# Kernel tuning notes

Hardware: AMD Instinct MI355X
Metric: run time of the kernel (lower is better)

## Reference

```python
import jax, jax.numpy as jnp
import numpy as np

HIDDEN = 1024
TYPE_SIZE = 1000
BATCH = 32
SEQLEN = 512


def setup_inputs() -> dict:
    key = jax.random.key(0)
    k1, k2, k3, k4, k5 = jax.random.split(key, 5)
    event_seqs = jax.random.randint(k1, (BATCH, SEQLEN), 0, TYPE_SIZE + 1)
    duration_seqs = jax.random.uniform(k2, (BATCH, SEQLEN), dtype=jnp.float32)
    # nn.Linear(2H, 7H): weight [7H, 2H], bias [7H]
    bound = 1.0 / np.sqrt(2 * HIDDEN)
    W_rec = jax.random.uniform(k3, (7 * HIDDEN, 2 * HIDDEN), minval=-bound, maxval=bound, dtype=jnp.float32)
    b_rec = jax.random.uniform(k4, (7 * HIDDEN,), minval=-bound, maxval=bound, dtype=jnp.float32)
    emb_table = jax.random.normal(k5, (TYPE_SIZE + 1, HIDDEN), dtype=jnp.float32)
    return {"event_seqs": event_seqs, "duration_seqs": duration_seqs,
            "emb_table": emb_table, "W_rec": W_rec, "b_rec": b_rec}


def _ctlstm_forward(event_seqs, duration_seqs, emb_table, W_rec, b_rec):
    # batch_first=True: transpose to [T, B]
    ev = event_seqs.T          # [T, B]
    dur = duration_seqs.T      # [T, B]
    H = emb_table.shape[1]
    x = emb_table[ev]          # [T, B, H]
    # NOTE: the original forward re-inits h_d/c_d/c_bar to zeros every timestep,
    # so feed = concat(emb_t, zeros) and c_tm1 = c_bar_tm1 = 0: fully parallel in T.
    # rec(feed) with zero h-half == x @ W_rec[:, :H].T + b_rec
    gates = jnp.einsum('tbh,gh->tbg', x, W_rec[:, :H]) + b_rec  # [T, B, 7H]
    gi, gf, gz, go, gib, gfb, gd = jnp.split(gates, 7, axis=-1)
    gi = jax.nn.sigmoid(gi)
    gz = jnp.tanh(gz)
    go = jax.nn.sigmoid(go)
    gib = jax.nn.sigmoid(gib)
    gd = jax.nn.softplus(gd)
    # c_tm1 = 0, c_bar_tm1 = 0
    c = gi * gz                # [T, B, H]
    c_bar = gib * gz           # [T, B, H]
    c_d = c_bar + (c - c_bar) * jnp.exp(-gd * dur[..., None])
    h_d = go * jnp.tanh(c_d)
    return jnp.stack((h_d, c, c_bar, go, gd))  # [5, T, B, H]


def reference(event_seqs, duration_seqs, emb_table, W_rec, b_rec):
    return _ctlstm_forward(event_seqs, duration_seqs, emb_table, W_rec, b_rec)
```

## Files before the change

### kernel.cpp

```cpp
#include <hip/hip_runtime.h>
#include <stdint.h>

#define HID    1024
#define TYPES  1001
#define MPAD   1024
#define NGATES 5120
#define BATCH  32
#define SEQLEN 512
#define TB     (BATCH * SEQLEN)
#define TBH    ((size_t)TB * HID)
#define GSTRIDE ((size_t)MPAD * HID)

typedef __attribute__((ext_vector_type(4))) float  f32x4;
typedef __attribute__((ext_vector_type(8))) __bf16 bf16x8;

__device__ __forceinline__ uint32_t f2bf(float f) {
    uint32_t u = __float_as_uint(f);
    return (u + 0x7FFFu + ((u >> 16) & 1u)) >> 16;
}

__device__ __forceinline__ int gate_off(int g) {
    return (g + (g >= 1) + (g >= 4)) << 10;
}

#define GLD16(gp, lp) __builtin_amdgcn_global_load_lds(                        \
    (const __attribute__((address_space(1))) void*)(uintptr_t)(gp),            \
    (__attribute__((address_space(3))) void*)(uint32_t)(uintptr_t)(lp),        \
    16, 0, 0)

__global__ __launch_bounds__(256) void convert_kernel(
    const float* __restrict__ emb, const float* __restrict__ Wrec,
    uint16_t* __restrict__ Ebf, uint16_t* __restrict__ Wbf)
{
    const int row = blockIdx.x;
    const int tid = threadIdx.x;
    const float* src;
    uint16_t* dst;
    if (row < TYPES) {
        src = emb + (size_t)row * HID;
        dst = Ebf + (size_t)row * HID;
    } else {
        const int n = row - TYPES;
        const int g = n >> 10;
        const int h = n & 1023;
        src = Wrec + (size_t)(gate_off(g) + h) * (2 * HID);
        dst = Wbf + (size_t)n * HID;
    }
    float4 v = ((const float4*)src)[tid];
    uint2 p;
    p.x = f2bf(v.x) | (f2bf(v.y) << 16);
    p.y = f2bf(v.z) | (f2bf(v.w) << 16);
    ((uint2*)dst)[tid] = p;
}

__global__ __launch_bounds__(256) void gemm_gates(
    const uint16_t* __restrict__ E, const uint16_t* __restrict__ W,
    const float* __restrict__ brec, float* __restrict__ G)
{
    __shared__ uint16_t As[128 * 32];
    __shared__ uint16_t Bs[128 * 32];
    const int tM = blockIdx.x;
    const int tN = blockIdx.y;
    const int t = threadIdx.x;
    const int wave = t >> 6;
    const int lane = t & 63;
    const int lane15 = lane & 15;
    const int quad = lane >> 4;
    const int m0 = (wave >> 1) * 64;
    const int n0 = (wave & 1) * 64;

    f32x4 acc[4][4] = {};

    const uint16_t* Ag = E + (size_t)(tM * 128 + (t >> 2)) * HID + (t & 3) * 8;
    const uint16_t* Bg = W + (size_t)(tN * 128 + (t >> 2)) * HID + (t & 3) * 8;
    uint16_t* Al = &As[(t >> 2) * 32 + (t & 3) * 8];
    uint16_t* Bl = &Bs[(t >> 2) * 32 + (t & 3) * 8];

    for (int k0 = 0; k0 < HID; k0 += 32) {
        GLD16(Ag + k0, Al);
        GLD16(Ag + k0 + (size_t)64 * HID, Al + 64 * 32);
        GLD16(Bg + k0, Bl);
        GLD16(Bg + k0 + (size_t)64 * HID, Bl + 64 * 32);
        __syncthreads();

        bf16x8 af[4], bfr[4];
        #pragma unroll
        for (int i = 0; i < 4; i++)
            af[i] = *(const bf16x8*)&As[(m0 + i * 16 + lane15) * 32 + quad * 8];
        #pragma unroll
        for (int i = 0; i < 4; i++)
            bfr[i] = *(const bf16x8*)&Bs[(n0 + i * 16 + lane15) * 32 + quad * 8];

        #pragma unroll
        for (int im = 0; im < 4; im++)
            #pragma unroll
            for (int in = 0; in < 4; in++)
                acc[im][in] = __builtin_amdgcn_mfma_f32_16x16x32_bf16(
                    af[im], bfr[in], acc[im][in], 0, 0, 0);
        __syncthreads();
    }

    #pragma unroll
    for (int in = 0; in < 4; in++) {
        const int n = tN * 128 + n0 + in * 16 + lane15;
        const int g = n >> 10;
        const int h = n & 1023;
        const float bias = brec[gate_off(g) + h];
        float* Gg = G + (size_t)g * GSTRIDE + h;
        #pragma unroll
        for (int im = 0; im < 4; im++) {
            const int mb = tM * 128 + m0 + im * 16 + quad * 4;
            #pragma unroll
            for (int r = 0; r < 4; r++) {
                const float v = acc[im][in][r] + bias;
                float o;
                if (g == 1) {
                    float e = __expf(2.f * v);
                    o = 1.f - 2.f / (e + 1.f);
                } else if (g == 4) {
                    o = fmaxf(v, 0.f) + log1pf(__expf(-fabsf(v)));
                } else {
                    o = 1.f / (1.f + __expf(-v));
                }
                Gg[(size_t)(mb + r) * HID] = o;
            }
        }
    }
}

__global__ __launch_bounds__(256) void expand_kernel(
    const int* __restrict__ ev, const float* __restrict__ dur,
    const float* __restrict__ G, float* __restrict__ out)
{
    const int tb = blockIdx.x;
    const int t = tb >> 5;
    const int b = tb & 31;
    const int src = b * SEQLEN + t;
    const int u = ev[src];
    const float d = dur[src];
    const int tid = threadIdx.x;

    const float* Gu = G + (size_t)u * HID;
    f32x4 gi  = *((const f32x4*)(Gu + 0 * GSTRIDE) + tid);
    f32x4 gz  = *((const f32x4*)(Gu + 1 * GSTRIDE) + tid);
    f32x4 go  = *((const f32x4*)(Gu + 2 * GSTRIDE) + tid);
    f32x4 gib = *((const f32x4*)(Gu + 3 * GSTRIDE) + tid);
    f32x4 gd  = *((const f32x4*)(Gu + 4 * GSTRIDE) + tid);

    f32x4 c, cb, hd;
    #pragma unroll
    for (int j = 0; j < 4; j++) {
        float ci  = gi[j] * gz[j];
        float cbi = gib[j] * gz[j];
        float e   = __expf(-gd[j] * d);
        float cdi = cbi + (ci - cbi) * e;
        float t2  = __expf(2.f * cdi);
        c[j]  = ci;
        cb[j] = cbi;
        hd[j] = go[j] * (1.f - 2.f / (t2 + 1.f));
    }

    float* o = out + (size_t)tb * HID;
    __builtin_nontemporal_store(hd, (f32x4*)(o + 0 * TBH) + tid);
    __builtin_nontemporal_store(c,  (f32x4*)(o + 1 * TBH) + tid);
    __builtin_nontemporal_store(cb, (f32x4*)(o + 2 * TBH) + tid);
    __builtin_nontemporal_store(go, (f32x4*)(o + 3 * TBH) + tid);
    __builtin_nontemporal_store(gd, (f32x4*)(o + 4 * TBH) + tid);
}

extern "C" void kernel_launch(void* const* d_in, const int* in_sizes, int n_in,
                              void* d_out, int out_size, void* d_ws, size_t ws_size,
                              hipStream_t stream) {
    const int*   ev   = (const int*)d_in[0];
    const float* dur  = (const float*)d_in[1];
    const float* emb  = (const float*)d_in[2];
    const float* Wrec = (const float*)d_in[3];
    const float* brec = (const float*)d_in[4];
    float* out = (float*)d_out;

    char* ws = (char*)d_ws;
    uint16_t* Ebf = (uint16_t*)ws;
    uint16_t* Wbf = (uint16_t*)(ws + (size_t)2 * 1024 * 1024);
    float*    G   = (float*)(ws + (size_t)12 * 1024 * 1024);

    convert_kernel<<<dim3(TYPES + NGATES), dim3(256), 0, stream>>>(emb, Wrec, Ebf, Wbf);
    gemm_gates<<<dim3(8, 40), dim3(256), 0, stream>>>(Ebf, Wbf, brec, G);
    expand_kernel<<<dim3(TB), dim3(256), 0, stream>>>(ev, dur, G, out);
}
```

Baseline: 466.0 us.

## Double-buffer GEMM with swizzled LDS, wider tiles, interleaved gate layout, 2-row expand

Rewrites the gate GEMM to use 128x160 tiles with BK=64, double-buffered LDS staging, and XOR-swizzled column placement to avoid bank conflicts, so the grid is 8x32 blocks. The gate table layout changes from gate-major to row-major interleaved, putting all five gates of one token contiguously. The expand kernel now processes two tokens per block. The aim is to cut GEMM load stalls and improve gather locality. The cost is more LDS and more registers per block, which may lower occupancy.

```diff
diff --git a/kernel.cpp b/kernel.cpp
--- a/kernel.cpp
+++ b/kernel.cpp
@@ -3,13 +3,15 @@
 
 #define HID    1024
 #define TYPES  1001
-#define MPAD   1024
 #define NGATES 5120
 #define BATCH  32
 #define SEQLEN 512
 #define TB     (BATCH * SEQLEN)
 #define TBH    ((size_t)TB * HID)
-#define GSTRIDE ((size_t)MPAD * HID)
+
+#define BK 64
+#define TM 128
+#define TN 160
 
 typedef __attribute__((ext_vector_type(4))) float  f32x4;
 typedef __attribute__((ext_vector_type(8))) __bf16 bf16x8;
@@ -57,61 +59,79 @@
     const uint16_t* __restrict__ E, const uint16_t* __restrict__ W,
     const float* __restrict__ brec, float* __restrict__ G)
 {
-    __shared__ uint16_t As[128 * 32];
-    __shared__ uint16_t Bs[128 * 32];
-    const int tM = blockIdx.x;
-    const int tN = blockIdx.y;
+    __shared__ uint16_t As[2][TM * BK];
+    __shared__ uint16_t Bs[2][TN * BK];
+    const int tMb = blockIdx.x;
+    const int tNb = blockIdx.y;
     const int t = threadIdx.x;
     const int wave = t >> 6;
     const int lane = t & 63;
     const int lane15 = lane & 15;
     const int quad = lane >> 4;
     const int m0 = (wave >> 1) * 64;
-    const int n0 = (wave & 1) * 64;
-
-    f32x4 acc[4][4] = {};
-
-    const uint16_t* Ag = E + (size_t)(tM * 128 + (t >> 2)) * HID + (t & 3) * 8;
-    const uint16_t* Bg = W + (size_t)(tN * 128 + (t >> 2)) * HID + (t & 3) * 8;
-    uint16_t* Al = &As[(t >> 2) * 32 + (t & 3) * 8];
-    uint16_t* Bl = &Bs[(t >> 2) * 32 + (t & 3) * 8];
-
-    for (int k0 = 0; k0 < HID; k0 += 32) {
-        GLD16(Ag + k0, Al);
-        GLD16(Ag + k0 + (size_t)64 * HID, Al + 64 * 32);
-        GLD16(Bg + k0, Bl);
-        GLD16(Bg + k0 + (size_t)64 * HID, Bl + 64 * 32);
+    const int n0 = (wave & 1) * 80;
+
+    const int rA = t >> 3;
+    const int csrc = (t & 7) ^ (rA & 7);
+    const uint16_t* Ag = E + (size_t)(tMb * TM + rA) * HID + csrc * 8;
+    const uint16_t* Bg = W + (size_t)(tNb * TN + rA) * HID + csrc * 8;
+
+    const int l7 = lane15 & 7;
+    const int pc0 = ((0 | quad) ^ l7) * 8;
+    const int pc1 = ((4 | quad) ^ l7) * 8;
+
+    f32x4 acc[4][5] = {};
+
+#define STAGE(buf, k0) do {                                                    \
+        _Pragma("unroll")                                                      \
+        for (int r = 0; r < 4; ++r)                                            \
+            GLD16(Ag + (k0) + (size_t)(r * 32) * HID, &As[buf][r * 2048 + t * 8]); \
+        _Pragma("unroll")                                                      \
+        for (int r = 0; r < 5; ++r)                                            \
+            GLD16(Bg + (k0) + (size_t)(r * 32) * HID, &Bs[buf][r * 2048 + t * 8]); \
+    } while (0)
+
+    STAGE(0, 0);
+    __syncthreads();
+
+    int cur = 0;
+    for (int kt = 0; kt < 16; ++kt) {
+        if (kt < 15) STAGE(cur ^ 1, (kt + 1) * BK);
+        const uint16_t* Ac = As[cur];
+        const uint16_t* Bc = Bs[cur];
+        #pragma unroll
+        for (int kk = 0; kk < 2; ++kk) {
+            const int pc = kk ? pc1 : pc0;
+            bf16x8 af[4], bv[5];
+            #pragma unroll
+            for (int im = 0; im < 4; ++im)
+                af[im] = *(const bf16x8*)&Ac[(m0 + im * 16 + lane15) * BK + pc];
+            #pragma unroll
+            for (int in = 0; in < 5; ++in)
+                bv[in] = *(const bf16x8*)&Bc[(n0 + in * 16 + lane15) * BK + pc];
+            #pragma unroll
+            for (int im = 0; im < 4; ++im)
+                #pragma unroll
+                for (int in = 0; in < 5; ++in)
+                    acc[im][in] = __builtin_amdgcn_mfma_f32_16x16x32_bf16(
+                        af[im], bv[in], acc[im][in], 0, 0, 0);
+        }
         __syncthreads();
-
-        bf16x8 af[4], bfr[4];
-        #pragma unroll
-        for (int i = 0; i < 4; i++)
-            af[i] = *(const bf16x8*)&As[(m0 + i * 16 + lane15) * 32 + quad * 8];
-        #pragma unroll
-        for (int i = 0; i < 4; i++)
-            bfr[i] = *(const bf16x8*)&Bs[(n0 + i * 16 + lane15) * 32 + quad * 8];
-
-        #pragma unroll
-        for (int im = 0; im < 4; im++)
-            #pragma unroll
-            for (int in = 0; in < 4; in++)
-                acc[im][in] = __builtin_amdgcn_mfma_f32_16x16x32_bf16(
-                    af[im], bfr[in], acc[im][in], 0, 0, 0);
-        __syncthreads();
-    }
+        cur ^= 1;
+    }
+#undef STAGE
 
     #pragma unroll
-    for (int in = 0; in < 4; in++) {
-        const int n = tN * 128 + n0 + in * 16 + lane15;
+    for (int in = 0; in < 5; ++in) {
+        const int n = tNb * TN + n0 + in * 16 + lane15;
         const int g = n >> 10;
         const int h = n & 1023;
         const float bias = brec[gate_off(g) + h];
-        float* Gg = G + (size_t)g * GSTRIDE + h;
         #pragma unroll
-        for (int im = 0; im < 4; im++) {
-            const int mb = tM * 128 + m0 + im * 16 + quad * 4;
-            #pragma unroll
-            for (int r = 0; r < 4; r++) {
+        for (int im = 0; im < 4; ++im) {
+            const int mb = tMb * TM + m0 + im * 16 + quad * 4;
+            #pragma unroll
+            for (int r = 0; r < 4; ++r) {
                 const float v = acc[im][in][r] + bias;
                 float o;
                 if (g == 1) {
@@ -122,7 +142,7 @@
                 } else {
                     o = 1.f / (1.f + __expf(-v));
                 }
-                Gg[(size_t)(mb + r) * HID] = o;
+                G[((size_t)(mb + r) * 5 + g) * HID + h] = o;
             }
         }
     }
@@ -132,40 +152,68 @@
     const int* __restrict__ ev, const float* __restrict__ dur,
     const float* __restrict__ G, float* __restrict__ out)
 {
-    const int tb = blockIdx.x;
-    const int t = tb >> 5;
-    const int b = tb & 31;
-    const int src = b * SEQLEN + t;
-    const int u = ev[src];
-    const float d = dur[src];
+    const int tb0 = blockIdx.x * 2;
+    const int tb1 = tb0 + 1;
     const int tid = threadIdx.x;
 
-    const float* Gu = G + (size_t)u * HID;
-    f32x4 gi  = *((const f32x4*)(Gu + 0 * GSTRIDE) + tid);
-    f32x4 gz  = *((const f32x4*)(Gu + 1 * GSTRIDE) + tid);
-    f32x4 go  = *((const f32x4*)(Gu + 2 * GSTRIDE) + tid);
-    f32x4 gib = *((const f32x4*)(Gu + 3 * GSTRIDE) + tid);
-    f32x4 gd  = *((const f32x4*)(Gu + 4 * GSTRIDE) + tid);
-
-    f32x4 c, cb, hd;
+    int s0, s1;
+    {
+        const int t0 = tb0 >> 5, b0 = tb0 & 31;
+        const int t1 = tb1 >> 5, b1 = tb1 & 31;
+        s0 = b0 * SEQLEN + t0;
+        s1 = b1 * SEQLEN + t1;
+    }
+    const int   u0 = ev[s0],  u1 = ev[s1];
+    const float d0 = dur[s0], d1 = dur[s1];
+
+    const float* Ga = G + (size_t)u0 * (5 * HID);
+    const float* Gb = G + (size_t)u1 * (5 * HID);
+
+    f32x4 gi0  = *((const f32x4*)(Ga + 0 * HID) + tid);
+    f32x4 gz0  = *((const f32x4*)(Ga + 1 * HID) + tid);
+    f32x4 go0  = *((const f32x4*)(Ga + 2 * HID) + tid);
+    f32x4 gib0 = *((const f32x4*)(Ga + 3 * HID) + tid);
+    f32x4 gd0  = *((const f32x4*)(Ga + 4 * HID) + tid);
+    f32x4 gi1  = *((const f32x4*)(Gb + 0 * HID) + tid);
+    f32x4 gz1  = *((const f32x4*)(Gb + 1 * HID) + tid);
+    f32x4 go1  = *((const f32x4*)(Gb + 2 * HID) + tid);
+    f32x4 gib1 = *((const f32x4*)(Gb + 3 * HID) + tid);
+    f32x4 gd1  = *((const f32x4*)(Gb + 4 * HID) + tid);
+
+    f32x4 c0, cb0, hd0, c1, cb1, hd1;
     #pragma unroll
-    for (int j = 0; j < 4; j++) {
-        float ci  = gi[j] * gz[j];
-        float cbi = gib[j] * gz[j];
-        float e   = __expf(-gd[j] * d);
+    for (int j = 0; j < 4; ++j) {
+        float ci  = gi0[j] * gz0[j];
+        float cbi = gib0[j] * gz0[j];
+        float e   = __expf(-gd0[j] * d0);
         float cdi = cbi + (ci - cbi) * e;
         float t2  = __expf(2.f * cdi);
-        c[j]  = ci;
-        cb[j] = cbi;
-        hd[j] = go[j] * (1.f - 2.f / (t2 + 1.f));
-    }
-
-    float* o = out + (size_t)tb * HID;
-    __builtin_nontemporal_store(hd, (f32x4*)(o + 0 * TBH) + tid);
-    __builtin_nontemporal_store(c,  (f32x4*)(o + 1 * TBH) + tid);
-    __builtin_nontemporal_store(cb, (f32x4*)(o + 2 * TBH) + tid);
-    __builtin_nontemporal_store(go, (f32x4*)(o + 3 * TBH) + tid);
-    __builtin_nontemporal_store(gd, (f32x4*)(o + 4 * TBH) + tid);
+        c0[j] = ci; cb0[j] = cbi;
+        hd0[j] = go0[j] * (1.f - 2.f / (t2 + 1.f));
+    }
+    #pragma unroll
+    for (int j = 0; j < 4; ++j) {
+        float ci  = gi1[j] * gz1[j];
+        float cbi = gib1[j] * gz1[j];
+        float e   = __expf(-gd1[j] * d1);
+        float cdi = cbi + (ci - cbi) * e;
+        float t2  = __expf(2.f * cdi);
+        c1[j] = ci; cb1[j] = cbi;
+        hd1[j] = go1[j] * (1.f - 2.f / (t2 + 1.f));
+    }
+
+    float* o0 = out + (size_t)tb0 * HID;
+    float* o1 = out + (size_t)tb1 * HID;
+    __builtin_nontemporal_store(hd0, (f32x4*)(o0 + 0 * TBH) + tid);
+    __builtin_nontemporal_store(c0,  (f32x4*)(o0 + 1 * TBH) + tid);
+    __builtin_nontemporal_store(cb0, (f32x4*)(o0 + 2 * TBH) + tid);
+    __builtin_nontemporal_store(go0, (f32x4*)(o0 + 3 * TBH) + tid);
+    __builtin_nontemporal_store(gd0, (f32x4*)(o0 + 4 * TBH) + tid);
+    __builtin_nontemporal_store(hd1, (f32x4*)(o1 + 0 * TBH) + tid);
+    __builtin_nontemporal_store(c1,  (f32x4*)(o1 + 1 * TBH) + tid);
+    __builtin_nontemporal_store(cb1, (f32x4*)(o1 + 2 * TBH) + tid);
+    __builtin_nontemporal_store(go1, (f32x4*)(o1 + 3 * TBH) + tid);
+    __builtin_nontemporal_store(gd1, (f32x4*)(o1 + 4 * TBH) + tid);
 }
 
 extern "C" void kernel_launch(void* const* d_in, const int* in_sizes, int n_in,
@@ -184,6 +232,6 @@
     float*    G   = (float*)(ws + (size_t)12 * 1024 * 1024);
 
     convert_kernel<<<dim3(TYPES + NGATES), dim3(256), 0, stream>>>(emb, Wrec, Ebf, Wbf);
-    gemm_gates<<<dim3(8, 40), dim3(256), 0, stream>>>(Ebf, Wbf, brec, G);
-    expand_kernel<<<dim3(TB), dim3(256), 0, stream>>>(ev, dur, G, out);
-}
+    gemm_gates<<<dim3(8, 32), dim3(256), 0, stream>>>(Ebf, Wbf, brec, G);
+    expand_kernel<<<dim3(TB / 2), dim3(256), 0, stream>>>(ev, dur, G, out);
+}
```

New measurement: 522.1 us. 12.0% more time.
